# Performance work log

Measured on AMD Instinct MI355X. Metric: run time of the kernel, lower is better.

## Reference

```python
import jax, jax.numpy as jnp
import numpy as np

N, D, I, O = 4096, 64, 512, 512  # samples, node_nums (bases), input_size, output_size


def setup_inputs() -> dict:
    key = jax.random.key(0)
    k1, k2, k3, k4 = jax.random.split(key, 4)
    # xavier_uniform bounds
    w_bound = float(np.sqrt(6.0 / (I + O)))
    b_bound = float(np.sqrt(6.0 / (D + O)))
    return {
        "x": jax.random.normal(k1, (N, I), dtype=jnp.float32),
        "var_vector": jax.random.uniform(k2, (N, D), dtype=jnp.float32),
        "W_1": jax.random.uniform(k3, (D, I, O), dtype=jnp.float32, minval=-w_bound, maxval=w_bound),
        "b_1": jax.random.uniform(k4, (D, O), dtype=jnp.float32, minval=-b_bound, maxval=b_bound),
    }


def reference(x, var_vector, W_1, b_1):
    # Math identical to: einsum('nd,dio->nio') then bmm(x[:,None,:], W)[:,0,:] + b.
    # Reordered contraction: contract x against each basis first (never forms n,i,o).
    y = jnp.einsum('ni,dio->ndo', x, W_1)        # [n, d, o]
    out = jnp.einsum('nd,ndo->no', var_vector, y)  # [n, o]
    b = jnp.einsum('nd,do->no', var_vector, b_1)   # [n, o]
    return out + b
```

## Files before the change

kernel.cpp:

```cpp
#include <hip/hip_runtime.h>
#include <hip/hip_bf16.h>
#include <stdint.h>
#include <stddef.h>

#define N_ 4096
#define D_ 64
#define I_ 512
#define O_ 512

#define BM 256
#define BN 128
#define SPLITS 4
#define DPG 16
#define PAIRS (DPG / 2)
#define KXS 16
#define NS (PAIRS * KXS)
#define SLOTA (128 * 128)
#define SLOTB (64 * 128)

typedef float  floatx4 __attribute__((ext_vector_type(4)));
typedef short  shortx8 __attribute__((ext_vector_type(8)));
typedef __bf16 bf16x8  __attribute__((ext_vector_type(8)));

__device__ __forceinline__ void gload_lds16(const void* g, void* l) {
  __builtin_amdgcn_global_load_lds(
      (const __attribute__((address_space(1))) void*)g,
      (__attribute__((address_space(3))) void*)l, 16, 0, 0);
}

__device__ __forceinline__ unsigned short f2bf(float f) {
  union { float f; unsigned int u; } c; c.f = f;
  unsigned int u = c.u;
  return (unsigned short)((u + 0x7fffu + ((u >> 16) & 1u)) >> 16);
}

__device__ __forceinline__ void mfma_bf16(floatx4& c, shortx8 a, shortx8 b) {
  union { shortx8 s; bf16x8 h; } ua, ub;
  ua.s = a; ub.s = b;
  c = __builtin_amdgcn_mfma_f32_16x16x32_bf16(ua.h, ub.h, c, 0, 0, 0);
}

__global__ void k_cvt_x(const float* __restrict__ x, unsigned short* __restrict__ xb) {
  int idx = (blockIdx.x * blockDim.x + threadIdx.x) * 8;
  floatx4 a = *(const floatx4*)(x + idx);
  floatx4 b = *(const floatx4*)(x + idx + 4);
  shortx8 o;
  o[0] = (short)f2bf(a[0]); o[1] = (short)f2bf(a[1]);
  o[2] = (short)f2bf(a[2]); o[3] = (short)f2bf(a[3]);
  o[4] = (short)f2bf(b[0]); o[5] = (short)f2bf(b[1]);
  o[6] = (short)f2bf(b[2]); o[7] = (short)f2bf(b[3]);
  *(shortx8*)(xb + idx) = o;
}

__global__ void k_cvt_w(const float* __restrict__ w, unsigned short* __restrict__ wt) {
  __shared__ unsigned short T[64][72];
  int bid = blockIdx.x;
  int d  = bid >> 6;
  int it = (bid >> 3) & 7;
  int ot = bid & 7;
  int i0 = it * 64, o0 = ot * 64;
  int t = threadIdx.x;
  const float* wp = w + ((size_t)d * I_ + i0) * O_ + o0;
  #pragma unroll
  for (int j = 0; j < 16; ++j) {
    int idx = j * 256 + t;
    int r = idx >> 6, c = idx & 63;
    T[r][c] = f2bf(wp[(size_t)r * O_ + c]);
  }
  __syncthreads();
  unsigned short* op = wt + ((size_t)d * O_ + o0) * I_ + i0;
  #pragma unroll
  for (int j = 0; j < 16; ++j) {
    int idx = j * 256 + t;
    int r = idx >> 6, c = idx & 63;
    op[(size_t)r * I_ + c] = T[c][r];
  }
}

__global__ void k_bias(const float* __restrict__ var, const float* __restrict__ b1,
                       float* __restrict__ out) {
  __shared__ float vs[16][64];
  int n0 = blockIdx.x * 16;
  int t = threadIdx.x;
  #pragma unroll
  for (int j = 0; j < 4; ++j) {
    int idx = j * 256 + t;
    vs[idx >> 6][idx & 63] = var[(size_t)n0 * D_ + idx];
  }
  __syncthreads();
  float a0[16], a1[16];
  #pragma unroll
  for (int r = 0; r < 16; ++r) { a0[r] = 0.f; a1[r] = 0.f; }
  for (int d = 0; d < D_; ++d) {
    float b0 = b1[(size_t)d * O_ + t];
    float bb = b1[(size_t)d * O_ + 256 + t];
    #pragma unroll
    for (int r = 0; r < 16; ++r) { a0[r] += vs[r][d] * b0; a1[r] += vs[r][d] * bb; }
  }
  #pragma unroll
  for (int r = 0; r < 16; ++r) {
    out[(size_t)(n0 + r) * O_ + t]       = a0[r];
    out[(size_t)(n0 + r) * O_ + 256 + t] = a1[r];
  }
}

__global__ __launch_bounds__(512) void k_gemm(
    const unsigned short* __restrict__ xb, const unsigned short* __restrict__ wt,
    const float* __restrict__ var, float* __restrict__ out) {
  __shared__ alignas(16) char lA[4][SLOTA];
  __shared__ alignas(16) char lB[4][2][SLOTB];
  __shared__ alignas(16) float lV[DPG * BM];

  const int tid = threadIdx.x;
  const int bid = blockIdx.x;
  const int g  = bid & 15;
  const int mt = bid >> 4;
  const int ot = g >> 2, split = g & 3;
  const int brow = mt * BM, bcol = ot * BN, d0 = split * DPG;

  const int lane = tid & 63, wid = tid >> 6;
  const int wr = wid >> 1, wc = wid & 1;
  const int l15 = lane & 15, l4 = lane >> 4;

  #pragma unroll
  for (int j = 0; j < (DPG * BM) / 512; ++j) {
    int idx = j * 512 + tid;
    int dd = idx >> 8, row = idx & (BM - 1);
    lV[idx] = var[(size_t)(brow + row) * D_ + d0 + dd];
  }

  const char* xbB = (const char*)xb;
  const char* wtB = (const char*)wt;

  int pbA[2]; size_t gbA[2];
  #pragma unroll
  for (int c = 0; c < 2; ++c) {
    int pb = (c * 512 + tid) << 4;
    int rl = pb >> 7;
    int colG = (pb & 127) ^ ((rl & 7) << 4);
    int r_src = rl + ((colG >> 6) << 7);
    int k_src = (colG & 63) >> 1;
    pbA[c] = pb;
    gbA[c] = ((size_t)(brow + r_src) * I_ + k_src) * 2;
  }
  int pbB; size_t gbB;
  {
    int pb = tid << 4;
    int rl = pb >> 7;
    int colG = (pb & 127) ^ ((rl & 7) << 4);
    int r_src = rl + ((colG >> 6) << 6);
    int k_src = (colG & 63) >> 1;
    pbB = pb;
    gbB = ((size_t)(bcol + r_src) * I_ + k_src) * 2;
  }

  int avOff[4], bvOff[4];
  #pragma unroll
  for (int m = 0; m < 4; ++m) {
    int r = wr * 64 + m * 16 + l15;
    int rl = r & 127;
    avOff[m] = rl * 128 + ((((r >> 7) << 6) + l4 * 16) ^ ((rl & 7) << 4));
  }
  #pragma unroll
  for (int n = 0; n < 4; ++n) {
    int r = wc * 64 + n * 16 + l15;
    int rl = r & 63;
    bvOff[n] = rl * 128 + (((wc << 6) + l4 * 16) ^ ((rl & 7) << 4));
  }

  auto stage_A = [&](int s) {
    const int kx = s & 15;
    char* la = (char*)&lA[s & 3][0];
    #pragma unroll
    for (int c = 0; c < 2; ++c)
      gload_lds16(xbB + gbA[c] + (size_t)kx * 64, la + pbA[c]);
  };
  auto stage_B = [&](int s) {
    const int d = d0 + 2 * (s >> 4);
    const int kx = s & 15;
    const char* src = wtB + (size_t)d * (I_ * O_ * 2) + gbB + (size_t)kx * 64;
    gload_lds16(src, (char*)&lB[s & 3][0][0] + pbB);
    gload_lds16(src + (size_t)(I_ * O_ * 2), (char*)&lB[s & 3][1][0] + pbB);
  };

  stage_A(0); stage_B(0); stage_A(1); stage_B(1);

  const floatx4 vzero = {0.f, 0.f, 0.f, 0.f};
  floatx4 master[4][4];
  #pragma unroll
  for (int m = 0; m < 4; ++m)
    #pragma unroll
    for (int n = 0; n < 4; ++n) master[m][n] = vzero;

  asm volatile("s_waitcnt vmcnt(4) lgkmcnt(0)" ::: "memory");
  __builtin_amdgcn_sched_barrier(0);
  __builtin_amdgcn_s_barrier();

  for (int p = 0; p < PAIRS; ++p) {
    floatx4 acc0[4][4], acc1[4][4];
    #pragma unroll
    for (int m = 0; m < 4; ++m)
      #pragma unroll
      for (int n = 0; n < 4; ++n) { acc0[m][n] = vzero; acc1[m][n] = vzero; }

    #pragma unroll 1
    for (int kx = 0; kx < KXS; ++kx) {
      const int s = p * KXS + kx;
      const char* aS  = (const char*)&lA[s & 3][0];
      const char* bS0 = (const char*)&lB[s & 3][0][0];
      const char* bS1 = (const char*)&lB[s & 3][1][0];
      shortx8 av[4], bv0[4], bv1[4];

      #pragma unroll
      for (int m = 0; m < 4; ++m) av[m] = *(const shortx8*)(aS + avOff[m]);
      #pragma unroll
      for (int n = 0; n < 4; ++n) bv0[n] = *(const shortx8*)(bS0 + bvOff[n]);
      #pragma unroll
      for (int n = 0; n < 4; ++n) bv1[n] = *(const shortx8*)(bS1 + bvOff[n]);
      if (s + 2 < NS) { stage_A(s + 2); stage_B(s + 2); }

      asm volatile("s_waitcnt lgkmcnt(4)" ::: "memory");
      __builtin_amdgcn_sched_barrier(0);
      __builtin_amdgcn_s_setprio(1);
      #pragma unroll
      for (int m = 0; m < 4; ++m)
        #pragma unroll
        for (int n = 0; n < 4; ++n) mfma_bf16(acc0[m][n], av[m], bv0[n]);
      __builtin_amdgcn_sched_barrier(0);
      asm volatile("s_waitcnt lgkmcnt(0)" ::: "memory");
      __builtin_amdgcn_sched_barrier(0);
      #pragma unroll
      for (int m = 0; m < 4; ++m)
        #pragma unroll
        for (int n = 0; n < 4; ++n) mfma_bf16(acc1[m][n], av[m], bv1[n]);
      __builtin_amdgcn_s_setprio(0);

      if (s + 2 < NS)      { asm volatile("s_waitcnt vmcnt(4)" ::: "memory"); }
      else if (s + 1 < NS) { asm volatile("s_waitcnt vmcnt(0)" ::: "memory"); }
      __builtin_amdgcn_s_barrier();
    }

    #pragma unroll
    for (int m = 0; m < 4; ++m) {
      int rbase = wr * 64 + m * 16 + l4 * 4;
      floatx4 v0 = *(const floatx4*)&lV[(2 * p) * BM + rbase];
      floatx4 v1 = *(const floatx4*)&lV[(2 * p + 1) * BM + rbase];
      #pragma unroll
      for (int n = 0; n < 4; ++n)
        #pragma unroll
        for (int r = 0; r < 4; ++r)
          master[m][n][r] += v0[r] * acc0[m][n][r] + v1[r] * acc1[m][n][r];
    }
  }

  #pragma unroll
  for (int m = 0; m < 4; ++m) {
    int row0 = brow + wr * 64 + m * 16 + l4 * 4;
    #pragma unroll
    for (int n = 0; n < 4; ++n) {
      int col = bcol + wc * 64 + n * 16 + l15;
      #pragma unroll
      for (int r = 0; r < 4; ++r)
        atomicAdd(out + (size_t)(row0 + r) * O_ + col, master[m][n][r]);
    }
  }
}

__global__ void k_naive(const float* __restrict__ x, const float* __restrict__ var,
                        const float* __restrict__ w, const float* __restrict__ b1,
                        float* __restrict__ out) {
  int n = blockIdx.x;
  int o = blockIdx.y * 128 + threadIdx.x;
  const float* xp = x + (size_t)n * I_;
  float acc = 0.f;
  for (int d = 0; d < D_; ++d) {
    const float* wp = w + (size_t)d * I_ * O_ + o;
    float y = 0.f;
    for (int i = 0; i < I_; ++i) y += xp[i] * wp[(size_t)i * O_];
    acc += var[(size_t)n * D_ + d] * (y + b1[(size_t)d * O_ + o]);
  }
  out[(size_t)n * O_ + o] = acc;
}

extern "C" void kernel_launch(void* const* d_in, const int* in_sizes, int n_in,
                              void* d_out, int out_size, void* d_ws, size_t ws_size,
                              hipStream_t stream) {
  const float* x   = (const float*)d_in[0];
  const float* var = (const float*)d_in[1];
  const float* W   = (const float*)d_in[2];
  const float* b1  = (const float*)d_in[3];
  float* out = (float*)d_out;

  const size_t wt_bytes = (size_t)D_ * I_ * O_ * 2;
  const size_t xb_bytes = (size_t)N_ * I_ * 2;
  if (ws_size >= wt_bytes + xb_bytes) {
    unsigned short* wt = (unsigned short*)d_ws;
    unsigned short* xb = (unsigned short*)((char*)d_ws + wt_bytes);
    k_cvt_x<<<dim3((N_ * I_) / (256 * 8)), dim3(256), 0, stream>>>(x, xb);
    k_cvt_w<<<dim3(D_ * 64), dim3(256), 0, stream>>>(W, wt);
    k_bias<<<dim3(N_ / 16), dim3(256), 0, stream>>>(var, b1, out);
    k_gemm<<<dim3((N_ / BM) * (O_ / BN) * SPLITS), dim3(512), 0, stream>>>(xb, wt, var, out);
  } else {
    k_naive<<<dim3(N_, O_ / 128), dim3(128), 0, stream>>>(x, var, W, b1, out);
  }
}
```

Before: 176.3 us.

## Merge preprocessing kernels into one launch and restructure GEMM inner-loop scheduling

Combines the x conversion, W conversion/transpose and bias kernels into a single block-indexed kernel, removing two launches and their serialization gaps. In the GEMM, the pair epilogue moves into the kx loop under a condition, the kx loop is unrolled by 4, and the outer loop is kept rolled. The manual lgkmcnt waits, sched barriers and setprio around the MFMAs are dropped, so the compiler's default scheduling replaces them. This risks worse MFMA/LDS overlap and higher register pressure in exchange for less loop overhead.

```diff
diff --git a/kernel.cpp b/kernel.cpp
--- a/kernel.cpp
+++ b/kernel.cpp
@@ -40,67 +40,69 @@
   c = __builtin_amdgcn_mfma_f32_16x16x32_bf16(ua.h, ub.h, c, 0, 0, 0);
 }
 
-__global__ void k_cvt_x(const float* __restrict__ x, unsigned short* __restrict__ xb) {
-  int idx = (blockIdx.x * blockDim.x + threadIdx.x) * 8;
-  floatx4 a = *(const floatx4*)(x + idx);
-  floatx4 b = *(const floatx4*)(x + idx + 4);
-  shortx8 o;
-  o[0] = (short)f2bf(a[0]); o[1] = (short)f2bf(a[1]);
-  o[2] = (short)f2bf(a[2]); o[3] = (short)f2bf(a[3]);
-  o[4] = (short)f2bf(b[0]); o[5] = (short)f2bf(b[1]);
-  o[6] = (short)f2bf(b[2]); o[7] = (short)f2bf(b[3]);
-  *(shortx8*)(xb + idx) = o;
-}
-
-__global__ void k_cvt_w(const float* __restrict__ w, unsigned short* __restrict__ wt) {
+__global__ __launch_bounds__(256) void k_pre(
+    const float* __restrict__ x, const float* __restrict__ W,
+    const float* __restrict__ var, const float* __restrict__ b1,
+    unsigned short* __restrict__ xb, unsigned short* __restrict__ wt,
+    float* __restrict__ out) {
   __shared__ unsigned short T[64][72];
-  int bid = blockIdx.x;
-  int d  = bid >> 6;
-  int it = (bid >> 3) & 7;
-  int ot = bid & 7;
-  int i0 = it * 64, o0 = ot * 64;
-  int t = threadIdx.x;
-  const float* wp = w + ((size_t)d * I_ + i0) * O_ + o0;
-  #pragma unroll
-  for (int j = 0; j < 16; ++j) {
-    int idx = j * 256 + t;
-    int r = idx >> 6, c = idx & 63;
-    T[r][c] = f2bf(wp[(size_t)r * O_ + c]);
-  }
-  __syncthreads();
-  unsigned short* op = wt + ((size_t)d * O_ + o0) * I_ + i0;
-  #pragma unroll
-  for (int j = 0; j < 16; ++j) {
-    int idx = j * 256 + t;
-    int r = idx >> 6, c = idx & 63;
-    op[(size_t)r * I_ + c] = T[c][r];
-  }
-}
-
-__global__ void k_bias(const float* __restrict__ var, const float* __restrict__ b1,
-                       float* __restrict__ out) {
   __shared__ float vs[16][64];
-  int n0 = blockIdx.x * 16;
-  int t = threadIdx.x;
-  #pragma unroll
-  for (int j = 0; j < 4; ++j) {
-    int idx = j * 256 + t;
-    vs[idx >> 6][idx & 63] = var[(size_t)n0 * D_ + idx];
-  }
-  __syncthreads();
-  float a0[16], a1[16];
-  #pragma unroll
-  for (int r = 0; r < 16; ++r) { a0[r] = 0.f; a1[r] = 0.f; }
-  for (int d = 0; d < D_; ++d) {
-    float b0 = b1[(size_t)d * O_ + t];
-    float bb = b1[(size_t)d * O_ + 256 + t];
-    #pragma unroll
-    for (int r = 0; r < 16; ++r) { a0[r] += vs[r][d] * b0; a1[r] += vs[r][d] * bb; }
-  }
-  #pragma unroll
-  for (int r = 0; r < 16; ++r) {
-    out[(size_t)(n0 + r) * O_ + t]       = a0[r];
-    out[(size_t)(n0 + r) * O_ + 256 + t] = a1[r];
+  const int b = blockIdx.x;
+  const int t = threadIdx.x;
+
+  if (b < 1024) {
+    int idx = (b * 256 + t) * 8;
+    floatx4 a = *(const floatx4*)(x + idx);
+    floatx4 c = *(const floatx4*)(x + idx + 4);
+    shortx8 o;
+    o[0] = (short)f2bf(a[0]); o[1] = (short)f2bf(a[1]);
+    o[2] = (short)f2bf(a[2]); o[3] = (short)f2bf(a[3]);
+    o[4] = (short)f2bf(c[0]); o[5] = (short)f2bf(c[1]);
+    o[6] = (short)f2bf(c[2]); o[7] = (short)f2bf(c[3]);
+    *(shortx8*)(xb + idx) = o;
+  } else if (b < 5120) {
+    int bid = b - 1024;
+    int d  = bid >> 6;
+    int it = (bid >> 3) & 7;
+    int ot = bid & 7;
+    int i0 = it * 64, o0 = ot * 64;
+    const float* wp = W + ((size_t)d * I_ + i0) * O_ + o0;
+    #pragma unroll
+    for (int j = 0; j < 16; ++j) {
+      int idx = j * 256 + t;
+      int r = idx >> 6, c = idx & 63;
+      T[r][c] = f2bf(wp[(size_t)r * O_ + c]);
+    }
+    __syncthreads();
+    unsigned short* op = wt + ((size_t)d * O_ + o0) * I_ + i0;
+    #pragma unroll
+    for (int j = 0; j < 16; ++j) {
+      int idx = j * 256 + t;
+      int r = idx >> 6, c = idx & 63;
+      op[(size_t)r * I_ + c] = T[c][r];
+    }
+  } else {
+    int n0 = (b - 5120) * 16;
+    #pragma unroll
+    for (int j = 0; j < 4; ++j) {
+      int idx = j * 256 + t;
+      vs[idx >> 6][idx & 63] = var[(size_t)n0 * D_ + idx];
+    }
+    __syncthreads();
+    float a0[16], a1[16];
+    #pragma unroll
+    for (int r = 0; r < 16; ++r) { a0[r] = 0.f; a1[r] = 0.f; }
+    for (int d = 0; d < D_; ++d) {
+      float b0 = b1[(size_t)d * O_ + t];
+      float bb = b1[(size_t)d * O_ + 256 + t];
+      #pragma unroll
+      for (int r = 0; r < 16; ++r) { a0[r] += vs[r][d] * b0; a1[r] += vs[r][d] * bb; }
+    }
+    #pragma unroll
+    for (int r = 0; r < 16; ++r) {
+      out[(size_t)(n0 + r) * O_ + t]       = a0[r];
+      out[(size_t)(n0 + r) * O_ + 256 + t] = a1[r];
+    }
   }
 }
 
@@ -196,6 +198,7 @@
   __builtin_amdgcn_sched_barrier(0);
   __builtin_amdgcn_s_barrier();
 
+  #pragma unroll 1
   for (int p = 0; p < PAIRS; ++p) {
     floatx4 acc0[4][4], acc1[4][4];
     #pragma unroll
@@ -203,7 +206,7 @@
       #pragma unroll
       for (int n = 0; n < 4; ++n) { acc0[m][n] = vzero; acc1[m][n] = vzero; }
 
-    #pragma unroll 1
+    #pragma unroll 4
     for (int kx = 0; kx < KXS; ++kx) {
       const int s = p * KXS + kx;
       const char* aS  = (const char*)&lA[s & 3][0];
@@ -219,37 +222,38 @@
       for (int n = 0; n < 4; ++n) bv1[n] = *(const shortx8*)(bS1 + bvOff[n]);
       if (s + 2 < NS) { stage_A(s + 2); stage_B(s + 2); }
 
-      asm volatile("s_waitcnt lgkmcnt(4)" ::: "memory");
-      __builtin_amdgcn_sched_barrier(0);
-      __builtin_amdgcn_s_setprio(1);
       #pragma unroll
       for (int m = 0; m < 4; ++m)
         #pragma unroll
         for (int n = 0; n < 4; ++n) mfma_bf16(acc0[m][n], av[m], bv0[n]);
-      __builtin_amdgcn_sched_barrier(0);
-      asm volatile("s_waitcnt lgkmcnt(0)" ::: "memory");
-      __builtin_amdgcn_sched_barrier(0);
       #pragma unroll
       for (int m = 0; m < 4; ++m)
         #pragma unroll
         for (int n = 0; n < 4; ++n) mfma_bf16(acc1[m][n], av[m], bv1[n]);
-      __builtin_amdgcn_s_setprio(0);
+
+      if ((s & 15) == 15) {
+        int pp = s >> 4;
+        #pragma unroll
+        for (int m = 0; m < 4; ++m) {
+          int rbase = wr * 64 + m * 16 + l4 * 4;
+          floatx4 v0 = *(const floatx4*)&lV[(2 * pp) * BM + rbase];
+          floatx4 v1 = *(const floatx4*)&lV[(2 * pp + 1) * BM + rbase];
+          #pragma unroll
+          for (int n = 0; n < 4; ++n)
+            #pragma unroll
+            for (int r = 0; r < 4; ++r) {
+              master[m][n][r] += v0[r] * acc0[m][n][r] + v1[r] * acc1[m][n][r];
+              acc0[m][n][r] = 0.f;
+              acc1[m][n][r] = 0.f;
+            }
+        }
+      }
 
       if (s + 2 < NS)      { asm volatile("s_waitcnt vmcnt(4)" ::: "memory"); }
       else if (s + 1 < NS) { asm volatile("s_waitcnt vmcnt(0)" ::: "memory"); }
+      __builtin_amdgcn_sched_barrier(0);
       __builtin_amdgcn_s_barrier();
-    }
-
-    #pragma unroll
-    for (int m = 0; m < 4; ++m) {
-      int rbase = wr * 64 + m * 16 + l4 * 4;
-      floatx4 v0 = *(const floatx4*)&lV[(2 * p) * BM + rbase];
-      floatx4 v1 = *(const floatx4*)&lV[(2 * p + 1) * BM + rbase];
-      #pragma unroll
-      for (int n = 0; n < 4; ++n)
-        #pragma unroll
-        for (int r = 0; r < 4; ++r)
-          master[m][n][r] += v0[r] * acc0[m][n][r] + v1[r] * acc1[m][n][r];
+      __builtin_amdgcn_sched_barrier(0);
     }
   }
 
@@ -296,9 +300,7 @@
   if (ws_size >= wt_bytes + xb_bytes) {
     unsigned short* wt = (unsigned short*)d_ws;
     unsigned short* xb = (unsigned short*)((char*)d_ws + wt_bytes);
-    k_cvt_x<<<dim3((N_ * I_) / (256 * 8)), dim3(256), 0, stream>>>(x, xb);
-    k_cvt_w<<<dim3(D_ * 64), dim3(256), 0, stream>>>(W, wt);
-    k_bias<<<dim3(N_ / 16), dim3(256), 0, stream>>>(var, b1, out);
+    k_pre<<<dim3(5376), dim3(256), 0, stream>>>(x, W, var, b1, xb, wt, out);
     k_gemm<<<dim3((N_ / BM) * (O_ / BN) * SPLITS), dim3(512), 0, stream>>>(xb, wt, var, out);
   } else {
     k_naive<<<dim3(N_, O_ / 128), dim3(128), 0, stream>>>(x, var, W, b1, out);
```

After: 230.5 us. 30.7% more time.
